# Optimization experiments

Hardware: AMD Instinct MI355X
Metric: run time of the kernel (lower is better)

The kernel has to match this reference:

```python
import jax, jax.numpy as jnp
import numpy as np

N = 100000
E = 1000000
D = 32          # numerical_dim
HID = 64        # hidden_dim
OUT = 1         # output_dim
REL = 4 * D     # relation feature dim
EPS = 1e-8


def setup_inputs() -> dict:
    key = jax.random.key(0)
    k_x, k_e, k_w1, k_b1, k_w2, k_b2 = jax.random.split(key, 6)
    x = jax.random.uniform(k_x, (N, D), dtype=jnp.float32)
    edge_index = jax.random.randint(k_e, (2, E), 0, N, dtype=jnp.int64)
    # Linear params (PyTorch convention: W [out, in], y = x @ W.T + b)
    lim1 = 1.0 / np.sqrt(REL)
    W1 = jax.random.uniform(k_w1, (HID, REL), minval=-lim1, maxval=lim1, dtype=jnp.float32)
    b1 = jax.random.uniform(k_b1, (HID,), minval=-lim1, maxval=lim1, dtype=jnp.float32)
    lim2 = 1.0 / np.sqrt(HID)
    W2 = jax.random.uniform(k_w2, (OUT, HID), minval=-lim2, maxval=lim2, dtype=jnp.float32)
    b2 = jax.random.uniform(k_b2, (OUT,), minval=-lim2, maxval=lim2, dtype=jnp.float32)
    return {"x": x, "edge_index": edge_index, "W1": W1, "b1": b1, "W2": W2, "b2": b2}


def _relation_features(x_i, x_j):
    ratio = x_i / (x_j + EPS)
    log_ratio = jnp.log(x_i + EPS) - jnp.log(x_j + EPS)
    abs_diff = jnp.abs(x_i - x_j)
    rel_diff = abs_diff / (jnp.maximum(x_i, x_j) + EPS)
    return jnp.concatenate([ratio, log_ratio, abs_diff, rel_diff], axis=-1)  # [E, 4D]


def reference(x, edge_index, W1, b1, W2, b2):
    src, dst = edge_index[0], edge_index[1]
    x_i = x[src]                      # [E, D] gather source node feats
    x_j = x[dst]                      # [E, D] gather target node feats
    rel = _relation_features(x_i, x_j)  # [E, 4D]
    h = jax.nn.relu(rel @ W1.T + b1)    # [E, HID]
    edge_bias = (h @ W2.T + b2).squeeze(-1)  # [E]
    return edge_bias
```

## Files before the change

kernel.cpp:

```cpp
#include <hip/hip_runtime.h>


#define DD    32
#define HID   64
#define RELF  128
#define EPSF  1e-8f

typedef short  bf16x8 __attribute__((ext_vector_type(8)));
typedef float  f32x4  __attribute__((ext_vector_type(4)));

union U8 { unsigned u[4]; bf16x8 v; };

static __device__ __forceinline__ unsigned pk_tr(float lo, float hi) {
    return __builtin_amdgcn_perm(__builtin_bit_cast(unsigned, hi),
                                 __builtin_bit_cast(unsigned, lo), 0x07060302u);
}
static __device__ __forceinline__ unsigned rne_bits(float f) {
    unsigned u = __builtin_bit_cast(unsigned, f);
    return u + 0x7fffu + ((u >> 16) & 1u);
}
static __device__ __forceinline__ unsigned pk_rne(float lo, float hi) {
    return __builtin_amdgcn_perm(rne_bits(hi), rne_bits(lo), 0x07060302u);
}
static __device__ __forceinline__ float hi_f32(float f) {
    return __builtin_bit_cast(float, __builtin_bit_cast(unsigned, f) & 0xffff0000u);
}

__global__ __launch_bounds__(256)
void prep_logx(const float* __restrict__ x, unsigned* __restrict__ lx, int nq)
{
    int i = blockIdx.x * blockDim.x + threadIdx.x;
    if (i >= nq) return;
    float4 v = ((const float4*)x)[i];
    uint2 o;
    o.x = pk_rne(__logf(v.x + EPSF), __logf(v.y + EPSF));
    o.y = pk_rne(__logf(v.z + EPSF), __logf(v.w + EPSF));
    ((uint2*)lx)[i] = o;
}

template <int PRE>
__global__ __launch_bounds__(256, 2)
void edge_bias_mfma(const float* __restrict__ x,
                    const int*   __restrict__ ei,
                    const float* __restrict__ W1,
                    const float* __restrict__ b1,
                    const float* __restrict__ W2,
                    const float* __restrict__ b2,
                    const short* __restrict__ lx,
                    float* __restrict__ out,
                    int E)
{
    const int lane = threadIdx.x & 63;
    const int wave = (blockIdx.x * blockDim.x + threadIdx.x) >> 6;
    const int nwv  = (gridDim.x * blockDim.x) >> 6;
    const int c = lane & 15;
    const int q = lane >> 4;

    bf16x8 W0h[4], W0l[4], WL[4], WLn[4], WA[4], WDm[4];
    #pragma unroll
    for (int nt = 0; nt < 4; ++nt) {
        const float* wr = W1 + (nt * 16 + c) * RELF + q * 8;
        U8 h, l, tt;
        #pragma unroll
        for (int p = 0; p < 4; ++p) {
            float w0 = wr[2 * p], w1 = wr[2 * p + 1];
            h.u[p] = pk_tr(w0, w1);
            l.u[p] = pk_rne(w0 - hi_f32(w0), w1 - hi_f32(w1));
        }
        W0h[nt] = h.v; W0l[nt] = l.v;
        #pragma unroll
        for (int p = 0; p < 4; ++p)
            tt.u[p] = pk_rne(wr[32 + 2 * p], wr[32 + 2 * p + 1]);
        WL[nt] = tt.v;
        #pragma unroll
        for (int p = 0; p < 4; ++p) tt.u[p] ^= 0x80008000u;
        WLn[nt] = tt.v;
        #pragma unroll
        for (int p = 0; p < 4; ++p)
            tt.u[p] = pk_rne(wr[64 + 2 * p], wr[64 + 2 * p + 1]);
        WA[nt] = tt.v;
        #pragma unroll
        for (int p = 0; p < 4; ++p)
            tt.u[p] = pk_rne(wr[96 + 2 * p], wr[96 + 2 * p + 1]);
        WDm[nt] = tt.v;
    }
    float b1v[4], w2v[4];
    #pragma unroll
    for (int nt = 0; nt < 4; ++nt) {
        b1v[nt] = b1[nt * 16 + c];
        w2v[nt] = W2[nt * 16 + c];
    }
    const float b2s = b2[0];

    const int ntiles = (E + 15) >> 4;
    int t = wave;
    if (t >= ntiles) return;

    auto ldidx = [&](int tt, int& s, int& d) {
        if (tt >= ntiles) tt = t;
        int em = (tt << 4) + c; if (em > E - 1) em = E - 1;
        s = ei[em]; d = ei[E + em];
    };
    auto gather = [&](int s, int d, float4& A0, float4& A1,
                      float4& B0, float4& B1, bf16x8& Li, bf16x8& Lj) {
        const float* pi = x + (long)s * DD + q * 8;
        const float* pj = x + (long)d * DD + q * 8;
        A0 = ((const float4*)pi)[0]; A1 = ((const float4*)pi)[1];
        B0 = ((const float4*)pj)[0]; B1 = ((const float4*)pj)[1];
        if constexpr (PRE) {
            Li = *(const bf16x8*)(lx + (long)s * DD + q * 8);
            Lj = *(const bf16x8*)(lx + (long)d * DD + q * 8);
        } else { (void)Li; (void)Lj; }
    };

    auto compute = [&](int tc, float4 xi0, float4 xi1, float4 xj0, float4 xj1,
                       bf16x8 aLi, bf16x8 aLj) {
        const int e0 = tc << 4;
        float xiv[8] = {xi0.x, xi0.y, xi0.z, xi0.w, xi1.x, xi1.y, xi1.z, xi1.w};
        float xjv[8] = {xj0.x, xj0.y, xj0.z, xj0.w, xj1.x, xj1.y, xj1.z, xj1.w};

        if constexpr (!PRE) {
            U8 ti, tj;
            #pragma unroll
            for (int p = 0; p < 4; ++p) {
                ti.u[p] = pk_rne(__logf(xiv[2*p] + EPSF), __logf(xiv[2*p+1] + EPSF));
                tj.u[p] = pk_rne(__logf(xjv[2*p] + EPSF), __logf(xjv[2*p+1] + EPSF));
            }
            aLi = ti.v; aLj = tj.v;
        }

        U8 R, Rl, Aa, Dd;
        #pragma unroll
        for (int p = 0; p < 4; ++p) {
            float a0 = xiv[2*p], a1 = xiv[2*p+1];
            float c0 = xjv[2*p], c1 = xjv[2*p+1];
            float r0 = a0 * __builtin_amdgcn_rcpf(c0 + EPSF);
            float r1 = a1 * __builtin_amdgcn_rcpf(c1 + EPSF);
            float d0 = fabsf(a0 - c0), d1 = fabsf(a1 - c1);
            float g0 = d0 * __builtin_amdgcn_rcpf(fmaxf(a0, c0) + EPSF);
            float g1 = d1 * __builtin_amdgcn_rcpf(fmaxf(a1, c1) + EPSF);
            R.u[p]  = pk_tr(r0, r1);
            Rl.u[p] = pk_tr(r0 - hi_f32(r0), r1 - hi_f32(r1));
            Aa.u[p] = pk_tr(d0, d1);
            Dd.u[p] = pk_tr(g0, g1);
        }

        f32x4 acc[4];
        #pragma unroll
        for (int nt = 0; nt < 4; ++nt) {
            acc[nt][0] = b1v[nt]; acc[nt][1] = b1v[nt];
            acc[nt][2] = b1v[nt]; acc[nt][3] = b1v[nt];
        }
        #pragma unroll
        for (int nt = 0; nt < 4; ++nt) {
            acc[nt] = __builtin_amdgcn_mfma_f32_16x16x32_bf16(R.v,  W0h[nt], acc[nt], 0, 0, 0);
            acc[nt] = __builtin_amdgcn_mfma_f32_16x16x32_bf16(Rl.v, W0h[nt], acc[nt], 0, 0, 0);
            acc[nt] = __builtin_amdgcn_mfma_f32_16x16x32_bf16(R.v,  W0l[nt], acc[nt], 0, 0, 0);
            acc[nt] = __builtin_amdgcn_mfma_f32_16x16x32_bf16(aLi,  WL[nt],  acc[nt], 0, 0, 0);
            acc[nt] = __builtin_amdgcn_mfma_f32_16x16x32_bf16(aLj,  WLn[nt], acc[nt], 0, 0, 0);
            acc[nt] = __builtin_amdgcn_mfma_f32_16x16x32_bf16(Aa.v, WA[nt],  acc[nt], 0, 0, 0);
            acc[nt] = __builtin_amdgcn_mfma_f32_16x16x32_bf16(Dd.v, WDm[nt], acc[nt], 0, 0, 0);
        }

        float p[4];
        #pragma unroll
        for (int r = 0; r < 4; ++r) {
            float pp = 0.f;
            #pragma unroll
            for (int nt = 0; nt < 4; ++nt)
                pp = fmaf(fmaxf(acc[nt][r], 0.f), w2v[nt], pp);
            pp += __shfl_xor(pp, 1);
            pp += __shfl_xor(pp, 2);
            pp += __shfl_xor(pp, 4);
            pp += __shfl_xor(pp, 8);
            p[r] = pp;
        }
        if (c < 4) {
            const int e = e0 + q * 4 + c;
            if (e < E) {
                float v = (c == 0) ? p[0] : (c == 1) ? p[1] : (c == 2) ? p[2] : p[3];
                out[e] = v + b2s;
            }
        }
    };

    float4 xA0, xA1, xA2, xA3; bf16x8 lA0, lA1;
    float4 xB0, xB1, xB2, xB3; bf16x8 lB0, lB1;
    int sC, dC;

    { int s, d; ldidx(t,           s, d); gather(s, d, xA0, xA1, xA2, xA3, lA0, lA1); }
    { int s, d; ldidx(t + nwv,     s, d); gather(s, d, xB0, xB1, xB2, xB3, lB0, lB1); }
    ldidx(t + 2 * nwv, sC, dC);

    for (;;) {
        compute(t, xA0, xA1, xA2, xA3, lA0, lA1);
        gather(sC, dC, xA0, xA1, xA2, xA3, lA0, lA1);
        ldidx(t + 3 * nwv, sC, dC);
        t += nwv; if (t >= ntiles) break;

        compute(t, xB0, xB1, xB2, xB3, lB0, lB1);
        gather(sC, dC, xB0, xB1, xB2, xB3, lB0, lB1);
        ldidx(t + 3 * nwv, sC, dC);
        t += nwv; if (t >= ntiles) break;
    }
}

extern "C" void kernel_launch(void* const* d_in, const int* in_sizes, int n_in,
                              void* d_out, int out_size, void* d_ws, size_t ws_size,
                              hipStream_t stream)
{
    const float* x   = (const float*)d_in[0];
    const int*   ei  = (const int*)  d_in[1];
    const float* W1  = (const float*)d_in[2];
    const float* b1  = (const float*)d_in[3];
    const float* W2  = (const float*)d_in[4];
    const float* b2  = (const float*)d_in[5];
    float* out = (float*)d_out;

    const int E  = out_size;
    const int Nd = in_sizes[0];
    short* lx = (short*)d_ws;

    const bool pre = ws_size >= (size_t)Nd * sizeof(short) && (Nd % 4) == 0;
    if (pre) {
        const int nq = Nd / 4;
        prep_logx<<<(nq + 255) / 256, 256, 0, stream>>>(x, (unsigned*)lx, nq);
        edge_bias_mfma<1><<<1024, 256, 0, stream>>>(x, ei, W1, b1, W2, b2, lx, out, E);
    } else {
        edge_bias_mfma<0><<<1024, 256, 0, stream>>>(x, ei, W1, b1, W2, b2, lx, out, E);
    }
}
```

Measured before the change: 147.6 us.

## Move W1 bf16 fragments to shared memory to raise occupancy

```diff
diff --git a/kernel.cpp b/kernel.cpp
--- a/kernel.cpp
+++ b/kernel.cpp
@@ -9,7 +9,7 @@
 typedef short  bf16x8 __attribute__((ext_vector_type(8)));
 typedef float  f32x4  __attribute__((ext_vector_type(4)));
 
-union U8 { unsigned u[4]; bf16x8 v; };
+union U8 { unsigned u[4]; bf16x8 v; uint4 q4; };
 
 static __device__ __forceinline__ unsigned pk_tr(float lo, float hi) {
     return __builtin_amdgcn_perm(__builtin_bit_cast(unsigned, hi),
@@ -39,7 +39,7 @@
 }
 
 template <int PRE>
-__global__ __launch_bounds__(256, 2)
+__global__ __launch_bounds__(256, 4)
 void edge_bias_mfma(const float* __restrict__ x,
                     const int*   __restrict__ ei,
                     const float* __restrict__ W1,
@@ -51,39 +51,39 @@
                     int E)
 {
     const int lane = threadIdx.x & 63;
+    const int wv   = threadIdx.x >> 6;
     const int wave = (blockIdx.x * blockDim.x + threadIdx.x) >> 6;
     const int nwv  = (gridDim.x * blockDim.x) >> 6;
     const int c = lane & 15;
     const int q = lane >> 4;
 
-    bf16x8 W0h[4], W0l[4], WL[4], WLn[4], WA[4], WDm[4];
-    #pragma unroll
-    for (int nt = 0; nt < 4; ++nt) {
-        const float* wr = W1 + (nt * 16 + c) * RELF + q * 8;
-        U8 h, l, tt;
-        #pragma unroll
-        for (int p = 0; p < 4; ++p) {
-            float w0 = wr[2 * p], w1 = wr[2 * p + 1];
-            h.u[p] = pk_tr(w0, w1);
-            l.u[p] = pk_rne(w0 - hi_f32(w0), w1 - hi_f32(w1));
-        }
-        W0h[nt] = h.v; W0l[nt] = l.v;
-        #pragma unroll
-        for (int p = 0; p < 4; ++p)
-            tt.u[p] = pk_rne(wr[32 + 2 * p], wr[32 + 2 * p + 1]);
-        WL[nt] = tt.v;
-        #pragma unroll
-        for (int p = 0; p < 4; ++p) tt.u[p] ^= 0x80008000u;
-        WLn[nt] = tt.v;
-        #pragma unroll
-        for (int p = 0; p < 4; ++p)
-            tt.u[p] = pk_rne(wr[64 + 2 * p], wr[64 + 2 * p + 1]);
-        WA[nt] = tt.v;
-        #pragma unroll
-        for (int p = 0; p < 4; ++p)
-            tt.u[p] = pk_rne(wr[96 + 2 * p], wr[96 + 2 * p + 1]);
-        WDm[nt] = tt.v;
-    }
+    __shared__ uint4 sW[20 * 64];
+    for (int s = wv; s < 5; s += 4) {
+        #pragma unroll
+        for (int nt = 0; nt < 4; ++nt) {
+            const float* wr = W1 + (nt * 16 + c) * RELF + q * 8;
+            U8 t;
+            if (s == 0) {
+                #pragma unroll
+                for (int p = 0; p < 4; ++p)
+                    t.u[p] = pk_tr(wr[2*p], wr[2*p+1]);
+            } else if (s == 1) {
+                #pragma unroll
+                for (int p = 0; p < 4; ++p) {
+                    float w0 = wr[2*p], w1 = wr[2*p+1];
+                    t.u[p] = pk_rne(w0 - hi_f32(w0), w1 - hi_f32(w1));
+                }
+            } else {
+                const int base = (s == 2) ? 32 : (s == 3) ? 64 : 96;
+                #pragma unroll
+                for (int p = 0; p < 4; ++p)
+                    t.u[p] = pk_rne(wr[base + 2*p], wr[base + 2*p + 1]);
+            }
+            sW[(s * 4 + nt) * 64 + lane] = t.q4;
+        }
+    }
+    __syncthreads();
+
     float b1v[4], w2v[4];
     #pragma unroll
     for (int nt = 0; nt < 4; ++nt) {
@@ -96,9 +96,9 @@
     int t = wave;
     if (t >= ntiles) return;
 
-    auto ldidx = [&](int tt, int& s, int& d) {
-        if (tt >= ntiles) tt = t;
-        int em = (tt << 4) + c; if (em > E - 1) em = E - 1;
+    auto ldidx = [&](int tt_, int& s, int& d) {
+        if (tt_ >= ntiles) tt_ = t;
+        int em = (tt_ << 4) + c; if (em > E - 1) em = E - 1;
         s = ei[em]; d = ei[E + em];
     };
     auto gather = [&](int s, int d, float4& A0, float4& A1,
@@ -115,7 +115,6 @@
 
     auto compute = [&](int tc, float4 xi0, float4 xi1, float4 xj0, float4 xj1,
                        bf16x8 aLi, bf16x8 aLj) {
-        const int e0 = tc << 4;
         float xiv[8] = {xi0.x, xi0.y, xi0.z, xi0.w, xi1.x, xi1.y, xi1.z, xi1.w};
         float xjv[8] = {xj0.x, xj0.y, xj0.z, xj0.w, xj1.x, xj1.y, xj1.z, xj1.w};
 
@@ -128,6 +127,9 @@
             }
             aLi = ti.v; aLj = tj.v;
         }
+        U8 nj; nj.v = aLj;
+        #pragma unroll
+        for (int p = 0; p < 4; ++p) nj.u[p] ^= 0x80008000u;
 
         U8 R, Rl, Aa, Dd;
         #pragma unroll
@@ -145,6 +147,13 @@
             Dd.u[p] = pk_tr(g0, g1);
         }
 
+        int off = lane;
+        asm volatile("" : "+v"(off));
+        auto ldfrag = [&](int s, int nt) {
+            U8 w; w.q4 = sW[(s * 4 + nt) * 64 + off];
+            return w.v;
+        };
+
         f32x4 acc[4];
         #pragma unroll
         for (int nt = 0; nt < 4; ++nt) {
@@ -153,13 +162,18 @@
         }
         #pragma unroll
         for (int nt = 0; nt < 4; ++nt) {
-            acc[nt] = __builtin_amdgcn_mfma_f32_16x16x32_bf16(R.v,  W0h[nt], acc[nt], 0, 0, 0);
-            acc[nt] = __builtin_amdgcn_mfma_f32_16x16x32_bf16(Rl.v, W0h[nt], acc[nt], 0, 0, 0);
-            acc[nt] = __builtin_amdgcn_mfma_f32_16x16x32_bf16(R.v,  W0l[nt], acc[nt], 0, 0, 0);
-            acc[nt] = __builtin_amdgcn_mfma_f32_16x16x32_bf16(aLi,  WL[nt],  acc[nt], 0, 0, 0);
-            acc[nt] = __builtin_amdgcn_mfma_f32_16x16x32_bf16(aLj,  WLn[nt], acc[nt], 0, 0, 0);
-            acc[nt] = __builtin_amdgcn_mfma_f32_16x16x32_bf16(Aa.v, WA[nt],  acc[nt], 0, 0, 0);
-            acc[nt] = __builtin_amdgcn_mfma_f32_16x16x32_bf16(Dd.v, WDm[nt], acc[nt], 0, 0, 0);
+            bf16x8 fW0h = ldfrag(0, nt);
+            bf16x8 fW0l = ldfrag(1, nt);
+            bf16x8 fWL  = ldfrag(2, nt);
+            bf16x8 fWA  = ldfrag(3, nt);
+            bf16x8 fWD  = ldfrag(4, nt);
+            acc[nt] = __builtin_amdgcn_mfma_f32_16x16x32_bf16(R.v,  fW0h, acc[nt], 0, 0, 0);
+            acc[nt] = __builtin_amdgcn_mfma_f32_16x16x32_bf16(Rl.v, fW0h, acc[nt], 0, 0, 0);
+            acc[nt] = __builtin_amdgcn_mfma_f32_16x16x32_bf16(R.v,  fW0l, acc[nt], 0, 0, 0);
+            acc[nt] = __builtin_amdgcn_mfma_f32_16x16x32_bf16(aLi,  fWL,  acc[nt], 0, 0, 0);
+            acc[nt] = __builtin_amdgcn_mfma_f32_16x16x32_bf16(nj.v, fWL,  acc[nt], 0, 0, 0);
+            acc[nt] = __builtin_amdgcn_mfma_f32_16x16x32_bf16(Aa.v, fWA,  acc[nt], 0, 0, 0);
+            acc[nt] = __builtin_amdgcn_mfma_f32_16x16x32_bf16(Dd.v, fWD,  acc[nt], 0, 0, 0);
         }
 
         float p[4];
@@ -176,7 +190,7 @@
             p[r] = pp;
         }
         if (c < 4) {
-            const int e = e0 + q * 4 + c;
+            const int e = (tc << 4) + q * 4 + c;
             if (e < E) {
                 float v = (c == 0) ? p[0] : (c == 1) ? p[1] : (c == 2) ? p[2] : p[3];
                 out[e] = v + b2s;
@@ -184,24 +198,24 @@
         }
     };
 
-    float4 xA0, xA1, xA2, xA3; bf16x8 lA0, lA1;
-    float4 xB0, xB1, xB2, xB3; bf16x8 lB0, lB1;
-    int sC, dC;
-
-    { int s, d; ldidx(t,           s, d); gather(s, d, xA0, xA1, xA2, xA3, lA0, lA1); }
-    { int s, d; ldidx(t + nwv,     s, d); gather(s, d, xB0, xB1, xB2, xB3, lB0, lB1); }
-    ldidx(t + 2 * nwv, sC, dC);
-
-    for (;;) {
-        compute(t, xA0, xA1, xA2, xA3, lA0, lA1);
-        gather(sC, dC, xA0, xA1, xA2, xA3, lA0, lA1);
-        ldidx(t + 3 * nwv, sC, dC);
-        t += nwv; if (t >= ntiles) break;
-
-        compute(t, xB0, xB1, xB2, xB3, lB0, lB1);
-        gather(sC, dC, xB0, xB1, xB2, xB3, lB0, lB1);
-        ldidx(t + 3 * nwv, sC, dC);
-        t += nwv; if (t >= ntiles) break;
+    float4 xi0C, xi1C, xj0C, xj1C;
+    bf16x8 LiC, LjC;
+    int srcN, dstN;
+    { int s, d; ldidx(t, s, d); gather(s, d, xi0C, xi1C, xj0C, xj1C, LiC, LjC); }
+    ldidx(t + nwv, srcN, dstN);
+
+    for (; t < ntiles; t += nwv) {
+        float4 xi0N, xi1N, xj0N, xj1N;
+        bf16x8 LiN, LjN;
+        gather(srcN, dstN, xi0N, xi1N, xj0N, xj1N, LiN, LjN);
+        int srcN2, dstN2;
+        ldidx(t + 2 * nwv, srcN2, dstN2);
+
+        compute(t, xi0C, xi1C, xj0C, xj1C, LiC, LjC);
+
+        xi0C = xi0N; xi1C = xi1N; xj0C = xj0N; xj1C = xj1N;
+        LiC = LiN; LjC = LjN;
+        srcN = srcN2; dstN = dstN2;
     }
 }
 
@@ -225,8 +239,8 @@
     if (pre) {
         const int nq = Nd / 4;
         prep_logx<<<(nq + 255) / 256, 256, 0, stream>>>(x, (unsigned*)lx, nq);
-        edge_bias_mfma<1><<<1024, 256, 0, stream>>>(x, ei, W1, b1, W2, b2, lx, out, E);
+        edge_bias_mfma<1><<<2048, 256, 0, stream>>>(x, ei, W1, b1, W2, b2, lx, out, E);
     } else {
-        edge_bias_mfma<0><<<1024, 256, 0, stream>>>(x, ei, W1, b1, W2, b2, lx, out, E);
-    }
-}
+        edge_bias_mfma<0><<<2048, 256, 0, stream>>>(x, ei, W1, b1, W2, b2, lx, out, E);
+    }
+}
```

New measurement: 143.4 us. 2.8% less time.
